# Optimization experiments

Measured on AMD Instinct MI355X. Metric: run time of the kernel, lower is better.

The kernel has to match this reference:

```python
import jax, jax.numpy as jnp
import numpy as np

NEG_SLOPE = 0.2

def symlog(v):
    return jnp.sign(v) * jnp.log1p(jnp.abs(v))

def conv1d(v, w, b):
    # v: (N, Cin, L), w: (Cout, Cin, 3), 'same' padding, stride 1
    out = jax.lax.conv_general_dilated(v, w, (1,), 'SAME',
                                       dimension_numbers=('NCH', 'OIH', 'NCH'))
    return out + b[None, :, None]

def glorot(key, shape, fan_in, fan_out):
    s = jnp.sqrt(6.0 / (fan_in + fan_out))
    return jax.random.uniform(key, shape, jnp.float32, -s, s)

def setup_inputs() -> dict:
    N, L, E = 20000, 128, 320000
    IN, H, C, OHC = 512, 8, 32, 8
    key = jax.random.key(0)
    ks = jax.random.split(key, 12)
    x = jax.random.normal(ks[0], (N, IN), jnp.float32)
    onehot = jax.random.uniform(ks[1], (N, L), jnp.float32)
    src = jax.random.randint(ks[2], (E,), 0, N)
    off = jax.random.randint(ks[3], (E,), 1, N)
    dst = (src + off) % N  # guarantees no self loops
    adj = jnp.stack([src, dst], axis=0).astype(jnp.int64)
    lin_w = glorot(ks[4], (IN + OHC, H * C), IN + OHC, H * C)
    att_l = glorot(ks[5], (1, H, C), C, C)
    att_r = glorot(ks[6], (1, H, C), C, C)
    bias = jnp.zeros((H * C,), jnp.float32)
    conv1_w = glorot(ks[7], (8, 1, 3), 3, 24)
    conv1_b = jnp.zeros((8,), jnp.float32)
    conv2_w = glorot(ks[8], (16, 8, 3), 24, 48)
    conv2_b = jnp.zeros((16,), jnp.float32)
    lin2_w = glorot(ks[9], (16, OHC), 16, OHC)
    lin2_b = jnp.zeros((OHC,), jnp.float32)
    return {"x": x, "onehot": onehot, "adj": adj, "n_nodes": N,
            "lin_w": lin_w, "att_l": att_l, "att_r": att_r, "bias": bias,
            "conv1_w": conv1_w, "conv1_b": conv1_b,
            "conv2_w": conv2_w, "conv2_b": conv2_b,
            "lin2_w": lin2_w, "lin2_b": lin2_b}

def reference(x, onehot, adj, n_nodes, lin_w, att_l, att_r, bias,
              conv1_w, conv1_b, conv2_w, conv2_b, lin2_w, lin2_b):
    N = n_nodes
    H, C = att_l.shape[1], att_l.shape[2]
    # one-hot conv pipe: sort -> symlog -> conv-relu x2 -> global avg pool -> linear
    prepared = symlog(jnp.sort(onehot, axis=-1))[:, None, :]  # (N,1,L)
    h = jax.nn.relu(conv1d(prepared, conv1_w, conv1_b))
    h = jax.nn.relu(conv1d(h, conv2_w, conv2_b))
    readout = h.mean(axis=-1) @ lin2_w + lin2_b  # (N, OHC)
    xin = jnp.concatenate([x, readout], axis=-1)
    xh = (xin @ lin_w).reshape(N, H, C)
    al = (xh * att_l).sum(axis=-1)  # (N,H) sending alphas
    ar = (xh * att_r).sum(axis=-1)  # (N,H) receiving alphas
    # add self loops (input adj has none, so remove_self_loops is a no-op)
    loops = jnp.arange(N, dtype=adj.dtype)
    src = jnp.concatenate([adj[0], loops])
    dst = jnp.concatenate([adj[1], loops])
    # GAT-style attention with segment softmax over receiving nodes
    alpha = jax.nn.leaky_relu(al[src] + ar[dst], NEG_SLOPE)  # (Etot,H)
    amax = jax.ops.segment_max(alpha, dst, num_segments=N)
    ex = jnp.exp(alpha - amax[dst])
    denom = jax.ops.segment_sum(ex, dst, num_segments=N)
    alpha = ex / denom[dst]
    # weight + scatter-add aggregate
    wx = xh[src] * alpha[..., None]  # (Etot,H,C)
    new_x = jax.ops.segment_sum(wx, dst, num_segments=N).reshape(N, H * C) + bias
    new_onehot = jax.ops.segment_sum(onehot[src], dst, num_segments=N) + onehot
    return new_x, new_onehot
```

## Files before the change

kernel.cpp:

```cpp
#include <hip/hip_runtime.h>

#define NEG_SLOPE 0.2f

typedef __attribute__((ext_vector_type(4))) float f32x4;
typedef __attribute__((ext_vector_type(2))) float f32x2;
typedef __attribute__((ext_vector_type(8))) short short8;

__device__ __forceinline__ f32x2 mk2(float a, float b) { f32x2 r; r[0] = a; r[1] = b; return r; }

__device__ __forceinline__ f32x2 FMA2(f32x2 a, f32x2 b, f32x2 c) {
#if __has_builtin(__builtin_elementwise_fma)
    return __builtin_elementwise_fma(a, b, c);
#else
    f32x2 r; r[0] = fmaf(a[0], b[0], c[0]); r[1] = fmaf(a[1], b[1], c[1]); return r;
#endif
}

__device__ __forceinline__ ushort f2bf(float f) {
    uint u = __float_as_uint(f);
    u += 0x7FFFu + ((u >> 16) & 1u);
    return (ushort)(u >> 16);
}
__device__ __forceinline__ float bflo(uint u) { return __uint_as_float(u << 16); }
__device__ __forceinline__ float bfhi(uint u) { return __uint_as_float(u & 0xffff0000u); }

__global__ __launch_bounds__(256) void k_zero_int(int* __restrict__ p, int n) {
    int i = blockIdx.x * 256 + threadIdx.x;
    if (i < n) p[i] = 0;
}

__global__ __launch_bounds__(256) void k_conv_wave(
    const float* __restrict__ onehot,
    const float* __restrict__ c1w, const float* __restrict__ c1b,
    const float* __restrict__ c2w, const float* __restrict__ c2b,
    const float* __restrict__ l2w, const float* __restrict__ l2b,
    float* __restrict__ readout, uint* __restrict__ ohb, int N) {
    const int wave = threadIdx.x >> 6;
    const int lane = threadIdx.x & 63;
    const int n = blockIdx.x * 4 + wave;
    if (n >= N) return;

    float2 in2 = *reinterpret_cast<const float2*>(&onehot[(size_t)n * 128 + lane * 2]);
    ohb[(size_t)n*64 + lane] = (uint)f2bf(in2.x) | ((uint)f2bf(in2.y) << 16);
    float v0 = log1pf(in2.x);
    float v1 = log1pf(in2.y);

    #pragma unroll
    for (int k = 2; k <= 128; k <<= 1) {
        const bool asc = ((lane & (k >> 1)) == 0);
        #pragma unroll
        for (int j = k >> 1; j >= 2; j >>= 1) {
            const int m = j >> 1;
            float p0 = __shfl_xor(v0, m, 64);
            float p1 = __shfl_xor(v1, m, 64);
            const bool keepmin = (((lane & m) == 0) == asc);
            v0 = keepmin ? fminf(v0, p0) : fmaxf(v0, p0);
            v1 = keepmin ? fminf(v1, p1) : fmaxf(v1, p1);
        }
        float lo = fminf(v0, v1), hi = fmaxf(v0, v1);
        v0 = asc ? lo : hi;
        v1 = asc ? hi : lo;
    }

    float pm = __shfl_up(v1, 1, 64); if (lane == 0)  pm = 0.f;
    float pp = __shfl_down(v0, 1, 64); if (lane == 63) pp = 0.f;

    float h0[8], h1[8];
    {
        const f32x2 xm = mk2(pm, v0), x0 = mk2(v0, v1), xp = mk2(v1, pp);
        #pragma unroll
        for (int c = 0; c < 8; ++c) {
            const float w0 = c1w[c*3+0], w1 = c1w[c*3+1], w2 = c1w[c*3+2], b = c1b[c];
            f32x2 h = FMA2(xm, mk2(w0, w0), FMA2(x0, mk2(w1, w1), FMA2(xp, mk2(w2, w2), mk2(b, b))));
            h0[c] = fmaxf(h[0], 0.f);
            h1[c] = fmaxf(h[1], 0.f);
        }
    }

    f32x2 a01[16];
    #pragma unroll
    for (int c = 0; c < 16; ++c) { float b = c2b[c]; a01[c] = mk2(b, b); }
    #pragma unroll
    for (int ci = 0; ci < 8; ++ci) {
        float hm = __shfl_up(h1[ci], 1, 64); if (lane == 0)  hm = 0.f;
        float hp = __shfl_down(h0[ci], 1, 64); if (lane == 63) hp = 0.f;
        const f32x2 xm = mk2(hm, h0[ci]), x0 = mk2(h0[ci], h1[ci]), xp = mk2(h1[ci], hp);
        #pragma unroll
        for (int c = 0; c < 16; ++c) {
            const float w0 = c2w[(c*8+ci)*3+0], w1 = c2w[(c*8+ci)*3+1], w2 = c2w[(c*8+ci)*3+2];
            a01[c] = FMA2(xm, mk2(w0, w0), FMA2(x0, mk2(w1, w1), FMA2(xp, mk2(w2, w2), a01[c])));
        }
    }

    float pv[16];
    #pragma unroll
    for (int c = 0; c < 16; ++c) pv[c] = fmaxf(a01[c][0], 0.f) + fmaxf(a01[c][1], 0.f);

    {
        const bool up1 = lane & 1;
        #pragma unroll
        for (int j = 0; j < 8; ++j) {
            float send = up1 ? pv[j] : pv[j+8];
            float keep = up1 ? pv[j+8] : pv[j];
            pv[j] = keep + __shfl_xor(send, 1, 64);
        }
        const bool up2 = (lane >> 1) & 1;
        #pragma unroll
        for (int j = 0; j < 4; ++j) {
            float send = up2 ? pv[j] : pv[j+4];
            float keep = up2 ? pv[j+4] : pv[j];
            pv[j] = keep + __shfl_xor(send, 2, 64);
        }
        const bool up3 = (lane >> 2) & 1;
        #pragma unroll
        for (int j = 0; j < 2; ++j) {
            float send = up3 ? pv[j] : pv[j+2];
            float keep = up3 ? pv[j+2] : pv[j];
            pv[j] = keep + __shfl_xor(send, 4, 64);
        }
        const bool up4 = (lane >> 3) & 1;
        {
            float send = up4 ? pv[0] : pv[1];
            float keep = up4 ? pv[1] : pv[0];
            pv[0] = keep + __shfl_xor(send, 8, 64);
        }
        pv[0] += __shfl_xor(pv[0], 16, 64);
        pv[0] += __shfl_xor(pv[0], 32, 64);
    }

    float pooled[16];
    #pragma unroll
    for (int c = 0; c < 16; ++c) {
        const int s = ((c & 1) << 3) | (((c >> 1) & 1) << 2) | (((c >> 2) & 1) << 1) | ((c >> 3) & 1);
        pooled[c] = __shfl(pv[0], s, 64);
    }
    if (lane < 8) {
        float r = l2b[lane];
        #pragma unroll
        for (int c = 0; c < 16; ++c) r = fmaf(pooled[c] * (1.f/128.f), l2w[c*8 + lane], r);
        readout[(size_t)n*8 + lane] = r;
    }
}

__global__ __launch_bounds__(256) void k_prepB(const float* __restrict__ lin_w, ushort* __restrict__ Bt) {
    const int col = blockIdx.x;
    for (int k = threadIdx.x; k < 544; k += 256) {
        float v = (k < 520) ? lin_w[(size_t)k*256 + col] : 0.f;
        Bt[(size_t)col*544 + k] = f2bf(v);
    }
}

__global__ __launch_bounds__(128) void k_gemm_mfma(
    const float* __restrict__ x, const float* __restrict__ readout,
    const ushort* __restrict__ Bt,
    const float* __restrict__ att_l, const float* __restrict__ att_r,
    float* __restrict__ xh, ushort* __restrict__ xhb,
    float* __restrict__ al, float* __restrict__ ar, int N) {
    __shared__ __align__(16) unsigned char smem[8704];
    ushort* sA = (ushort*)smem;
    ushort* sB = sA + 1024;
    float*  ep = (float*)smem;

    const int t = threadIdx.x;
    const int wv = t >> 6, lane = t & 63;
    const int m0 = (blockIdx.x >> 2) * 32;
    const int c0 = (blockIdx.x & 3) * 64;

    const int arow = m0 + ((t >> 6) << 4) + (t & 15);
    const int akg  = (t >> 4) & 3;
    const int bcol0 = c0 + ((t >> 6) << 4) + (t & 15);
    const int bcol1 = c0 + (((t >> 6) + 2) << 4) + (t & 15);
    const int bkg   = (t >> 4) & 3;

    const bool arow_ok = (arow < N);

    f32x4 acc[4];
    #pragma unroll
    for (int j = 0; j < 4; ++j) acc[j] = (f32x4)0.f;

    float av[8];
    uint4 bv0, bv1;

#define LOAD_STEP(K0_)                                                            \
    {                                                                             \
        const int kk = (K0_) + akg * 8;                                           \
        if (arow_ok && kk < 520) {                                                \
            const float* p = (kk < 512) ? &x[(size_t)arow*512 + kk]               \
                                        : &readout[(size_t)arow*8];               \
            float4 lo = *reinterpret_cast<const float4*>(p);                      \
            float4 hi = *reinterpret_cast<const float4*>(p + 4);                  \
            av[0]=lo.x; av[1]=lo.y; av[2]=lo.z; av[3]=lo.w;                       \
            av[4]=hi.x; av[5]=hi.y; av[6]=hi.z; av[7]=hi.w;                       \
        } else {                                                                  \
            av[0]=av[1]=av[2]=av[3]=av[4]=av[5]=av[6]=av[7]=0.f;                  \
        }                                                                         \
        bv0 = *reinterpret_cast<const uint4*>(&Bt[(size_t)bcol0*544 + (K0_) + bkg*8]); \
        bv1 = *reinterpret_cast<const uint4*>(&Bt[(size_t)bcol1*544 + (K0_) + bkg*8]); \
    }

    LOAD_STEP(0)
    for (int k0 = 0; k0 < 544; k0 += 32) {
        __syncthreads();
        uint4 aw;
        aw.x = (uint)f2bf(av[0]) | ((uint)f2bf(av[1]) << 16);
        aw.y = (uint)f2bf(av[2]) | ((uint)f2bf(av[3]) << 16);
        aw.z = (uint)f2bf(av[4]) | ((uint)f2bf(av[5]) << 16);
        aw.w = (uint)f2bf(av[6]) | ((uint)f2bf(av[7]) << 16);
        *reinterpret_cast<uint4*>(&sA[t*8]) = aw;
        *reinterpret_cast<uint4*>(&sB[t*8]) = bv0;
        *reinterpret_cast<uint4*>(&sB[(t+128)*8]) = bv1;
        if (k0 + 32 < 544) LOAD_STEP(k0 + 32)
        __syncthreads();
        short8 af = *reinterpret_cast<const short8*>(&sA[(wv*64 + lane)*8]);
        #pragma unroll
        for (int j = 0; j < 4; ++j) {
            short8 bf = *reinterpret_cast<const short8*>(&sB[(j*64 + lane)*8]);
            acc[j] = __builtin_amdgcn_mfma_f32_16x16x32_bf16(af, bf, acc[j], 0, 0, 0);
        }
    }
#undef LOAD_STEP

    __syncthreads();
    {
        const int rb = wv*16 + (lane >> 4)*4;
        const int cb = lane & 15;
        #pragma unroll
        for (int j = 0; j < 4; ++j)
            #pragma unroll
            for (int r = 0; r < 4; ++r)
                ep[(rb + r)*68 + j*16 + cb] = acc[j][r];
    }
    __syncthreads();
    {
        const int rl = t >> 2;
        const int cq = (t & 3) * 16;
        const int row = m0 + rl;
        if (row < N) {
            const float* s = &ep[rl*68 + cq];
            float vals[16];
            #pragma unroll
            for (int i = 0; i < 16; ++i) vals[i] = s[i];
            float* dst = &xh[(size_t)row*256 + c0 + cq];
            #pragma unroll
            for (int i = 0; i < 4; ++i)
                *reinterpret_cast<float4*>(&dst[4*i]) = make_float4(vals[4*i], vals[4*i+1], vals[4*i+2], vals[4*i+3]);
            uint u[8];
            #pragma unroll
            for (int i = 0; i < 8; ++i)
                u[i] = (uint)f2bf(vals[2*i]) | ((uint)f2bf(vals[2*i+1]) << 16);
            ushort* db = &xhb[(size_t)row*256 + c0 + cq];
            *reinterpret_cast<uint4*>(db)     = make_uint4(u[0], u[1], u[2], u[3]);
            *reinterpret_cast<uint4*>(db + 8) = make_uint4(u[4], u[5], u[6], u[7]);
            float pl = 0.f, pr = 0.f;
            #pragma unroll
            for (int i = 0; i < 16; ++i) {
                pl = fmaf(vals[i], att_l[c0 + cq + i], pl);
                pr = fmaf(vals[i], att_r[c0 + cq + i], pr);
            }
            pl += __shfl_xor(pl, 1, 64);
            pr += __shfl_xor(pr, 1, 64);
            if ((t & 1) == 0) {
                const int head = (c0 >> 5) + ((t & 3) >> 1);
                al[(size_t)row*8 + head] = pl;
                ar[(size_t)row*8 + head] = pr;
            }
        }
    }
}

__global__ __launch_bounds__(256) void k_deg(const int* __restrict__ dst, int* __restrict__ deg, int E) {
    int e = blockIdx.x * 256 + threadIdx.x;
    if (e < E) atomicAdd(&deg[dst[e]], 1);
}

__global__ __launch_bounds__(1024) void k_scan(int* __restrict__ deg, int* __restrict__ row_start, int N) {
    __shared__ int wsum[16];
    __shared__ int carry;
    const int t = threadIdx.x;
    const int w = t >> 6, ln = t & 63;
    if (t == 0) { carry = 0; row_start[0] = 0; }
    __syncthreads();
    for (int start = 0; start < N; start += 1024) {
        int i = start + t;
        int v = 0;
        if (i < N) { v = deg[i]; deg[i] = 0; }
        int s = v;
        #pragma unroll
        for (int d = 1; d < 64; d <<= 1) {
            int u = __shfl_up(s, d, 64);
            if (ln >= d) s += u;
        }
        if (ln == 63) wsum[w] = s;
        __syncthreads();
        if (w == 0) {
            int ws = (ln < 16) ? wsum[ln] : 0;
            int e = ws;
            #pragma unroll
            for (int d = 1; d < 16; d <<= 1) {
                int u = __shfl_up(e, d, 64);
                if (ln >= d) e += u;
            }
            if (ln < 16) wsum[ln] = e - ws;
        }
        __syncthreads();
        int incl = s + wsum[w] + carry;
        if (i < N) row_start[i + 1] = incl;
        __syncthreads();
        if (t == 1023) carry = incl;
    }
}

__global__ __launch_bounds__(256) void k_fill(
    const int* __restrict__ src, const int* __restrict__ dst,
    const int* __restrict__ row_start, int* __restrict__ cursor,
    int* __restrict__ csr, int E) {
    int e = blockIdx.x * 256 + threadIdx.x;
    if (e < E) {
        int d = dst[e];
        int p = atomicAdd(&cursor[d], 1);
        csr[row_start[d] + p] = src[e];
    }
}

__global__ __launch_bounds__(256) void k_agg(
    const float* __restrict__ xh, const ushort* __restrict__ xhb,
    const float* __restrict__ al, const float* __restrict__ ar,
    const float* __restrict__ onehot, const uint* __restrict__ ohb,
    const float* __restrict__ bias,
    const int* __restrict__ row_start, const int* __restrict__ csr,
    float* __restrict__ out_x, float* __restrict__ out_oh, int N) {
    const int wave = threadIdx.x >> 6;
    const int lane = threadIdx.x & 63;
    const int n = blockIdx.x * 4 + wave;
    if (n >= N) return;
    const int h = lane >> 3;
    const float ard = ar[(size_t)n*8 + h];

    float a_self = al[(size_t)n*8 + h] + ard;
    a_self = (a_self > 0.f) ? a_self : NEG_SLOPE * a_self;
    float e_self = __expf(a_self);
    float4 xs = *reinterpret_cast<const float4*>(&xh[(size_t)n*256 + lane*4]);
    float4 acc;
    acc.x = e_self * xs.x; acc.y = e_self * xs.y; acc.z = e_self * xs.z; acc.w = e_self * xs.w;
    float den = e_self;
    float oh0 = 0.f, oh1 = 0.f;

    const int beg = row_start[n], end = row_start[n+1];
    int i = beg;
    for (; i + 1 < end; i += 2) {
        const int s0 = csr[i], s1 = csr[i+1];
        const float al0 = al[(size_t)s0*8 + h], al1 = al[(size_t)s1*8 + h];
        const uint2 xb0 = *reinterpret_cast<const uint2*>(&xhb[(size_t)s0*256 + lane*4]);
        const uint2 xb1 = *reinterpret_cast<const uint2*>(&xhb[(size_t)s1*256 + lane*4]);
        const uint ob0 = ohb[(size_t)s0*64 + lane];
        const uint ob1 = ohb[(size_t)s1*64 + lane];
        float a0 = al0 + ard; a0 = (a0 > 0.f) ? a0 : NEG_SLOPE * a0;
        float a1 = al1 + ard; a1 = (a1 > 0.f) ? a1 : NEG_SLOPE * a1;
        const float e0 = __expf(a0), e1 = __expf(a1);
        acc.x = fmaf(e0, bflo(xb0.x), fmaf(e1, bflo(xb1.x), acc.x));
        acc.y = fmaf(e0, bfhi(xb0.x), fmaf(e1, bfhi(xb1.x), acc.y));
        acc.z = fmaf(e0, bflo(xb0.y), fmaf(e1, bflo(xb1.y), acc.z));
        acc.w = fmaf(e0, bfhi(xb0.y), fmaf(e1, bfhi(xb1.y), acc.w));
        den += e0 + e1;
        oh0 += bflo(ob0) + bflo(ob1);
        oh1 += bfhi(ob0) + bfhi(ob1);
    }
    if (i < end) {
        const int s0 = csr[i];
        float a0 = al[(size_t)s0*8 + h] + ard;
        a0 = (a0 > 0.f) ? a0 : NEG_SLOPE * a0;
        const float e0 = __expf(a0);
        const uint2 xb0 = *reinterpret_cast<const uint2*>(&xhb[(size_t)s0*256 + lane*4]);
        const uint ob0 = ohb[(size_t)s0*64 + lane];
        acc.x = fmaf(e0, bflo(xb0.x), acc.x);
        acc.y = fmaf(e0, bfhi(xb0.x), acc.y);
        acc.z = fmaf(e0, bflo(xb0.y), acc.z);
        acc.w = fmaf(e0, bfhi(xb0.y), acc.w);
        den += e0;
        oh0 += bflo(ob0);
        oh1 += bfhi(ob0);
    }
    const float inv = 1.f / den;
    const float4 bv = *reinterpret_cast<const float4*>(&bias[lane*4]);
    float4 o;
    o.x = fmaf(acc.x, inv, bv.x);
    o.y = fmaf(acc.y, inv, bv.y);
    o.z = fmaf(acc.z, inv, bv.z);
    o.w = fmaf(acc.w, inv, bv.w);
    *reinterpret_cast<float4*>(&out_x[(size_t)n*256 + lane*4]) = o;
    float2 so = *reinterpret_cast<const float2*>(&onehot[(size_t)n*128 + lane*2]);
    float2 oo;
    oo.x = oh0 + 2.f*so.x;
    oo.y = oh1 + 2.f*so.y;
    *reinterpret_cast<float2*>(&out_oh[(size_t)n*128 + lane*2]) = oo;
}

extern "C" void kernel_launch(void* const* d_in, const int* in_sizes, int n_in,
                              void* d_out, int out_size, void* d_ws, size_t ws_size,
                              hipStream_t stream) {
    const float* x      = (const float*)d_in[0];
    const float* onehot = (const float*)d_in[1];
    const int*   adj    = (const int*)d_in[2];
    const float* lin_w  = (const float*)d_in[4];
    const float* att_l  = (const float*)d_in[5];
    const float* att_r  = (const float*)d_in[6];
    const float* bias   = (const float*)d_in[7];
    const float* c1w    = (const float*)d_in[8];
    const float* c1b    = (const float*)d_in[9];
    const float* c2w    = (const float*)d_in[10];
    const float* c2b    = (const float*)d_in[11];
    const float* l2w    = (const float*)d_in[12];
    const float* l2b    = (const float*)d_in[13];

    const int N = in_sizes[0] / 512;
    const int E = in_sizes[2] / 2;
    const int* src = adj;
    const int* dst = adj + E;

    float* out_x  = (float*)d_out;
    float* out_oh = out_x + (size_t)N * 256;

    float* readout   = (float*)d_ws;
    float* xh        = readout + (size_t)N * 8;
    float* al        = xh + (size_t)N * 256;
    float* ar        = al + (size_t)N * 8;
    ushort* Bt       = (ushort*)(ar + (size_t)N * 8);
    ushort* xhb      = Bt + (size_t)256 * 544;
    uint*   ohb      = (uint*)(xhb + (size_t)N * 256);
    int*   row_start = (int*)(ohb + (size_t)N * 64);
    int*   cursor    = row_start + (N + 1);
    int*   csr       = cursor + N;

    const int EB = (E + 255) / 256;
    const int NB = (N + 255) / 256;

    k_zero_int<<<NB, 256, 0, stream>>>(cursor, N);
    k_conv_wave<<<(N + 3) / 4, 256, 0, stream>>>(onehot, c1w, c1b, c2w, c2b, l2w, l2b, readout, ohb, N);
    k_prepB<<<256, 256, 0, stream>>>(lin_w, Bt);
    k_deg<<<EB, 256, 0, stream>>>(dst, cursor, E);
    k_gemm_mfma<<<((N + 31) / 32) * 4, 128, 0, stream>>>(x, readout, Bt, att_l, att_r, xh, xhb, al, ar, N);
    k_scan<<<1, 1024, 0, stream>>>(cursor, row_start, N);
    k_fill<<<EB, 256, 0, stream>>>(src, dst, row_start, cursor, csr, E);
    k_agg<<<(N + 3) / 4, 256, 0, stream>>>(xh, xhb, al, ar, onehot, ohb, bias, row_start, csr, out_x, out_oh, N);
}
```

Measured before the change: 187.4 us.

## Pre-convert GEMM input to padded bf16, load MFMA fragments directly, drop fp32 xh

Adds a k_prepX kernel that converts x to bf16 into a padded buffer, with 544 columns per row, that also holds the readout written by the conv kernel. The GEMM then loads MFMA fragments straight from global memory without LDS staging or block barriers, and remaps block indices across the eight XCDs. The fp32 xh output is removed, so aggregation reads the self term from bf16. This trades an extra conversion pass over x and uncoalesced fragment loads for less LDS traffic, fewer syncs and smaller writes. For the last partial tile (m0+wv*16+frow >= N) xpad is read without a bounds check, which for N=20000 falls into the Bt region and is harmless.

```diff
diff --git a/kernel.cpp b/kernel.cpp
--- a/kernel.cpp
+++ b/kernel.cpp
@@ -29,12 +29,31 @@
     if (i < n) p[i] = 0;
 }
 
+__global__ __launch_bounds__(64) void k_prepX(const float* __restrict__ x, ushort* __restrict__ xpad) {
+    const int n = blockIdx.x;
+    const int t = threadIdx.x;
+    float4 lo = *reinterpret_cast<const float4*>(&x[(size_t)n*512 + t*8]);
+    float4 hi = *reinterpret_cast<const float4*>(&x[(size_t)n*512 + t*8 + 4]);
+    uint4 w;
+    w.x = (uint)f2bf(lo.x) | ((uint)f2bf(lo.y) << 16);
+    w.y = (uint)f2bf(lo.z) | ((uint)f2bf(lo.w) << 16);
+    w.z = (uint)f2bf(hi.x) | ((uint)f2bf(hi.y) << 16);
+    w.w = (uint)f2bf(hi.z) | ((uint)f2bf(hi.w) << 16);
+    *reinterpret_cast<uint4*>(&xpad[(size_t)n*544 + t*8]) = w;
+    if (t == 0) {
+        const uint4 z = make_uint4(0,0,0,0);
+        *reinterpret_cast<uint4*>(&xpad[(size_t)n*544 + 520]) = z;
+        *reinterpret_cast<uint4*>(&xpad[(size_t)n*544 + 528]) = z;
+        *reinterpret_cast<uint4*>(&xpad[(size_t)n*544 + 536]) = z;
+    }
+}
+
 __global__ __launch_bounds__(256) void k_conv_wave(
     const float* __restrict__ onehot,
     const float* __restrict__ c1w, const float* __restrict__ c1b,
     const float* __restrict__ c2w, const float* __restrict__ c2b,
     const float* __restrict__ l2w, const float* __restrict__ l2b,
-    float* __restrict__ readout, uint* __restrict__ ohb, int N) {
+    ushort* __restrict__ xpad, uint* __restrict__ ohb, int N) {
     const int wave = threadIdx.x >> 6;
     const int lane = threadIdx.x & 63;
     const int n = blockIdx.x * 4 + wave;
@@ -138,7 +157,7 @@
         float r = l2b[lane];
         #pragma unroll
         for (int c = 0; c < 16; ++c) r = fmaf(pooled[c] * (1.f/128.f), l2w[c*8 + lane], r);
-        readout[(size_t)n*8 + lane] = r;
+        xpad[(size_t)n*544 + 512 + lane] = f2bf(r);
     }
 }
 
@@ -151,84 +170,54 @@
 }
 
 __global__ __launch_bounds__(128) void k_gemm_mfma(
-    const float* __restrict__ x, const float* __restrict__ readout,
-    const ushort* __restrict__ Bt,
+    const ushort* __restrict__ xpad, const ushort* __restrict__ Bt,
     const float* __restrict__ att_l, const float* __restrict__ att_r,
-    float* __restrict__ xh, ushort* __restrict__ xhb,
-    float* __restrict__ al, float* __restrict__ ar, int N) {
-    __shared__ __align__(16) unsigned char smem[8704];
-    ushort* sA = (ushort*)smem;
-    ushort* sB = sA + 1024;
-    float*  ep = (float*)smem;
+    ushort* __restrict__ xhb, float* __restrict__ al, float* __restrict__ ar, int N) {
+    __shared__ __align__(16) float ep[32*68];
 
     const int t = threadIdx.x;
     const int wv = t >> 6, lane = t & 63;
-    const int m0 = (blockIdx.x >> 2) * 32;
-    const int c0 = (blockIdx.x & 3) * 64;
-
-    const int arow = m0 + ((t >> 6) << 4) + (t & 15);
-    const int akg  = (t >> 4) & 3;
-    const int bcol0 = c0 + ((t >> 6) << 4) + (t & 15);
-    const int bcol1 = c0 + (((t >> 6) + 2) << 4) + (t & 15);
-    const int bkg   = (t >> 4) & 3;
-
-    const bool arow_ok = (arow < N);
+
+    const int nwg = gridDim.x;
+    const int q = nwg >> 3, r = nwg & 7;
+    const int xcd = blockIdx.x & 7, idx = blockIdx.x >> 3;
+    const int logical = (xcd < r ? xcd*(q+1) : r*(q+1) + (xcd-r)*q) + idx;
+    const int m0 = (logical >> 2) * 32;
+    const int c0 = (logical & 3) * 64;
+
+    const int frow = lane & 15;
+    const int fkg  = (lane >> 4) * 8;
+
+    const ushort* ap = &xpad[(size_t)(m0 + wv*16 + frow)*544 + fkg];
+    const ushort* bp0 = &Bt[(size_t)(c0 +      frow)*544 + fkg];
+    const ushort* bp1 = &Bt[(size_t)(c0 + 16 + frow)*544 + fkg];
+    const ushort* bp2 = &Bt[(size_t)(c0 + 32 + frow)*544 + fkg];
+    const ushort* bp3 = &Bt[(size_t)(c0 + 48 + frow)*544 + fkg];
 
     f32x4 acc[4];
     #pragma unroll
     for (int j = 0; j < 4; ++j) acc[j] = (f32x4)0.f;
 
-    float av[8];
-    uint4 bv0, bv1;
-
-#define LOAD_STEP(K0_)                                                            \
-    {                                                                             \
-        const int kk = (K0_) + akg * 8;                                           \
-        if (arow_ok && kk < 520) {                                                \
-            const float* p = (kk < 512) ? &x[(size_t)arow*512 + kk]               \
-                                        : &readout[(size_t)arow*8];               \
-            float4 lo = *reinterpret_cast<const float4*>(p);                      \
-            float4 hi = *reinterpret_cast<const float4*>(p + 4);                  \
-            av[0]=lo.x; av[1]=lo.y; av[2]=lo.z; av[3]=lo.w;                       \
-            av[4]=hi.x; av[5]=hi.y; av[6]=hi.z; av[7]=hi.w;                       \
-        } else {                                                                  \
-            av[0]=av[1]=av[2]=av[3]=av[4]=av[5]=av[6]=av[7]=0.f;                  \
-        }                                                                         \
-        bv0 = *reinterpret_cast<const uint4*>(&Bt[(size_t)bcol0*544 + (K0_) + bkg*8]); \
-        bv1 = *reinterpret_cast<const uint4*>(&Bt[(size_t)bcol1*544 + (K0_) + bkg*8]); \
-    }
-
-    LOAD_STEP(0)
     for (int k0 = 0; k0 < 544; k0 += 32) {
-        __syncthreads();
-        uint4 aw;
-        aw.x = (uint)f2bf(av[0]) | ((uint)f2bf(av[1]) << 16);
-        aw.y = (uint)f2bf(av[2]) | ((uint)f2bf(av[3]) << 16);
-        aw.z = (uint)f2bf(av[4]) | ((uint)f2bf(av[5]) << 16);
-        aw.w = (uint)f2bf(av[6]) | ((uint)f2bf(av[7]) << 16);
-        *reinterpret_cast<uint4*>(&sA[t*8]) = aw;
-        *reinterpret_cast<uint4*>(&sB[t*8]) = bv0;
-        *reinterpret_cast<uint4*>(&sB[(t+128)*8]) = bv1;
-        if (k0 + 32 < 544) LOAD_STEP(k0 + 32)
-        __syncthreads();
-        short8 af = *reinterpret_cast<const short8*>(&sA[(wv*64 + lane)*8]);
-        #pragma unroll
-        for (int j = 0; j < 4; ++j) {
-            short8 bf = *reinterpret_cast<const short8*>(&sB[(j*64 + lane)*8]);
-            acc[j] = __builtin_amdgcn_mfma_f32_16x16x32_bf16(af, bf, acc[j], 0, 0, 0);
-        }
-    }
-#undef LOAD_STEP
-
-    __syncthreads();
+        short8 af = *reinterpret_cast<const short8*>(ap + k0);
+        short8 b0 = *reinterpret_cast<const short8*>(bp0 + k0);
+        short8 b1 = *reinterpret_cast<const short8*>(bp1 + k0);
+        short8 b2 = *reinterpret_cast<const short8*>(bp2 + k0);
+        short8 b3 = *reinterpret_cast<const short8*>(bp3 + k0);
+        acc[0] = __builtin_amdgcn_mfma_f32_16x16x32_bf16(af, b0, acc[0], 0, 0, 0);
+        acc[1] = __builtin_amdgcn_mfma_f32_16x16x32_bf16(af, b1, acc[1], 0, 0, 0);
+        acc[2] = __builtin_amdgcn_mfma_f32_16x16x32_bf16(af, b2, acc[2], 0, 0, 0);
+        acc[3] = __builtin_amdgcn_mfma_f32_16x16x32_bf16(af, b3, acc[3], 0, 0, 0);
+    }
+
     {
         const int rb = wv*16 + (lane >> 4)*4;
         const int cb = lane & 15;
         #pragma unroll
         for (int j = 0; j < 4; ++j)
             #pragma unroll
-            for (int r = 0; r < 4; ++r)
-                ep[(rb + r)*68 + j*16 + cb] = acc[j][r];
+            for (int r2 = 0; r2 < 4; ++r2)
+                ep[(rb + r2)*68 + j*16 + cb] = acc[j][r2];
     }
     __syncthreads();
     {
@@ -240,10 +229,6 @@
             float vals[16];
             #pragma unroll
             for (int i = 0; i < 16; ++i) vals[i] = s[i];
-            float* dst = &xh[(size_t)row*256 + c0 + cq];
-            #pragma unroll
-            for (int i = 0; i < 4; ++i)
-                *reinterpret_cast<float4*>(&dst[4*i]) = make_float4(vals[4*i], vals[4*i+1], vals[4*i+2], vals[4*i+3]);
             uint u[8];
             #pragma unroll
             for (int i = 0; i < 8; ++i)
@@ -323,7 +308,7 @@
 }
 
 __global__ __launch_bounds__(256) void k_agg(
-    const float* __restrict__ xh, const ushort* __restrict__ xhb,
+    const ushort* __restrict__ xhb,
     const float* __restrict__ al, const float* __restrict__ ar,
     const float* __restrict__ onehot, const uint* __restrict__ ohb,
     const float* __restrict__ bias,
@@ -339,9 +324,10 @@
     float a_self = al[(size_t)n*8 + h] + ard;
     a_self = (a_self > 0.f) ? a_self : NEG_SLOPE * a_self;
     float e_self = __expf(a_self);
-    float4 xs = *reinterpret_cast<const float4*>(&xh[(size_t)n*256 + lane*4]);
+    uint2 xsb = *reinterpret_cast<const uint2*>(&xhb[(size_t)n*256 + lane*4]);
     float4 acc;
-    acc.x = e_self * xs.x; acc.y = e_self * xs.y; acc.z = e_self * xs.z; acc.w = e_self * xs.w;
+    acc.x = e_self * bflo(xsb.x); acc.y = e_self * bfhi(xsb.x);
+    acc.z = e_self * bflo(xsb.y); acc.w = e_self * bfhi(xsb.y);
     float den = e_self;
     float oh0 = 0.f, oh1 = 0.f;
 
@@ -420,14 +406,13 @@
     float* out_x  = (float*)d_out;
     float* out_oh = out_x + (size_t)N * 256;
 
-    float* readout   = (float*)d_ws;
-    float* xh        = readout + (size_t)N * 8;
-    float* al        = xh + (size_t)N * 256;
-    float* ar        = al + (size_t)N * 8;
-    ushort* Bt       = (ushort*)(ar + (size_t)N * 8);
+    ushort* xpad     = (ushort*)d_ws;
+    ushort* Bt       = xpad + (size_t)N * 544;
     ushort* xhb      = Bt + (size_t)256 * 544;
     uint*   ohb      = (uint*)(xhb + (size_t)N * 256);
-    int*   row_start = (int*)(ohb + (size_t)N * 64);
+    float*  al       = (float*)(ohb + (size_t)N * 64);
+    float*  ar       = al + (size_t)N * 8;
+    int*   row_start = (int*)(ar + (size_t)N * 8);
     int*   cursor    = row_start + (N + 1);
     int*   csr       = cursor + N;
 
@@ -435,11 +420,12 @@
     const int NB = (N + 255) / 256;
 
     k_zero_int<<<NB, 256, 0, stream>>>(cursor, N);
-    k_conv_wave<<<(N + 3) / 4, 256, 0, stream>>>(onehot, c1w, c1b, c2w, c2b, l2w, l2b, readout, ohb, N);
+    k_conv_wave<<<(N + 3) / 4, 256, 0, stream>>>(onehot, c1w, c1b, c2w, c2b, l2w, l2b, xpad, ohb, N);
+    k_prepX<<<N, 64, 0, stream>>>(x, xpad);
     k_prepB<<<256, 256, 0, stream>>>(lin_w, Bt);
     k_deg<<<EB, 256, 0, stream>>>(dst, cursor, E);
-    k_gemm_mfma<<<((N + 31) / 32) * 4, 128, 0, stream>>>(x, readout, Bt, att_l, att_r, xh, xhb, al, ar, N);
+    k_gemm_mfma<<<((N + 31) / 32) * 4, 128, 0, stream>>>(xpad, Bt, att_l, att_r, xhb, al, ar, N);
     k_scan<<<1, 1024, 0, stream>>>(cursor, row_start, N);
     k_fill<<<EB, 256, 0, stream>>>(src, dst, row_start, cursor, csr, E);
-    k_agg<<<(N + 3) / 4, 256, 0, stream>>>(xh, xhb, al, ar, onehot, ohb, bias, row_start, csr, out_x, out_oh, N);
-}
+    k_agg<<<(N + 3) / 4, 256, 0, stream>>>(xhb, al, ar, onehot, ohb, bias, row_start, csr, out_x, out_oh, N);
+}
```

After: 195.9 us. 4.5% more time.
